# Kernel tuning notes

Measured on AMD Instinct MI355X. Metric: run time of the kernel, lower is better.

Reference implementation:

```python
import jax, jax.numpy as jnp
import numpy as np

N = 25000        # nodes
E = 400000       # edges (avg degree 16)
F = 128          # num_features
NRBF = 20        # num_rbf_features
CUTOFF = 5.0


def setup_inputs() -> dict:
    key = jax.random.key(0)
    ks = jax.random.split(key, 9)
    node_scalar = jax.random.normal(ks[0], (N, F), jnp.float32)
    node_vector = jax.random.normal(ks[1], (N, F, 3), jnp.float32)
    dst = jax.random.randint(ks[2], (E,), 0, N)
    src = jax.random.randint(ks[3], (E,), 0, N)
    r = jax.random.normal(ks[4], (E, 3), jnp.float32) * 1.5
    d = jnp.clip(jnp.linalg.norm(r, axis=-1), 0.1, None)
    adj_matrix = jnp.concatenate(
        [dst[:, None].astype(jnp.float32), src[:, None].astype(jnp.float32), r, d[:, None]],
        axis=-1)  # [E, 6]
    s_in = 1.0 / np.sqrt(F)
    s_rbf = 1.0 / np.sqrt(NRBF)
    W1 = jax.random.normal(ks[5], (F, F), jnp.float32) * s_in
    b1 = jnp.zeros((F,), jnp.float32)
    W2 = jax.random.normal(ks[6], (F, 3 * F), jnp.float32) * s_in
    b2 = jnp.zeros((3 * F,), jnp.float32)
    Wr = jax.random.normal(ks[7], (NRBF, 3 * F), jnp.float32) * s_rbf
    br = jnp.zeros((3 * F,), jnp.float32)
    return dict(node_scalar=node_scalar, node_vector=node_vector, adj_matrix=adj_matrix,
                W1=W1, b1=b1, W2=W2, b2=b2, Wr=Wr, br=br)


def reference(node_scalar, node_vector, adj_matrix, W1, b1, W2, b2, Wr, br):
    # scalar message MLP: Linear -> SiLU -> Linear, [N, 3F]
    atom_scalar = jax.nn.silu(node_scalar @ W1 + b1) @ W2 + b2

    dst = adj_matrix[:, 0].astype(jnp.int32)
    src = adj_matrix[:, 1].astype(jnp.int32)
    r_ij = adj_matrix[:, 2:5]              # [E, 3]
    d = adj_matrix[:, 5]                   # [E]

    # sinc expansion: sin(d * n * pi / cutoff) / d, n = 1..NRBF -> [E, NRBF]
    n_vals = jnp.arange(1, NRBF + 1, dtype=jnp.float32)
    sinc = jnp.sin(d[:, None] * n_vals * jnp.pi / CUTOFF) / d[:, None]
    rbf = sinc @ Wr + br                   # [E, 3F]
    cut = jnp.where(d < CUTOFF, 0.5 * (jnp.cos(jnp.pi * d / CUTOFF) + 1.0), 0.0)
    w = rbf * cut[:, None]                 # [E, 3F]

    pre_split = atom_scalar[src] * w       # [E, 3F]
    s1, s2, s3 = jnp.split(pre_split, 3, axis=-1)  # each [E, F]

    r_hat = r_ij / d[:, None]              # [E, 3]
    # message_vector: [E, F, 3]
    message_vector = node_vector[src] * s1[:, :, None] + s3[:, :, None] * r_hat[:, None, :]

    delta_s = jnp.zeros_like(node_scalar).at[dst].add(s2)
    delta_v = jnp.zeros_like(node_vector).at[dst].add(message_vector)
    return node_scalar + delta_s, node_vector + delta_v
```

## Files before the change

### kernel.cpp

```cpp
#include <hip/hip_runtime.h>

#define FDIM 128
#define NRBF 20
constexpr float CUTOFF_F = 5.0f;
constexpr float PI_F = 3.14159265358979323846f;

typedef _Float16 h2 __attribute__((ext_vector_type(2)));
typedef _Float16 half4 __attribute__((ext_vector_type(4)));
typedef float f32x4 __attribute__((ext_vector_type(4)));

__device__ __forceinline__ uint packh(float a, float b) {
  union { _Float16 h[2]; uint u; } x;
  x.h[0] = (_Float16)a;
  x.h[1] = (_Float16)b;
  return x.u;
}
__device__ __forceinline__ float h_lo(uint w) {
  union { uint u; _Float16 h[2]; } x;
  x.u = w;
  return (float)x.h[0];
}
__device__ __forceinline__ float h_hi(uint w) {
  union { uint u; _Float16 h[2]; } x;
  x.u = w;
  return (float)x.h[1];
}
__device__ __forceinline__ float dot2(uint cw, h2 w, float acc) {
#if __has_builtin(__builtin_amdgcn_fdot2)
  h2 c = __builtin_bit_cast(h2, cw);
  return __builtin_amdgcn_fdot2(c, w, acc, false);
#else
  return fmaf(h_hi(cw), (float)w[1], fmaf(h_lo(cw), (float)w[0], acc));
#endif
}

__global__ __launch_bounds__(256) void wconv2(const float* __restrict__ W1,
                                              const float* __restrict__ W2,
                                              _Float16* __restrict__ w1h,
                                              _Float16* __restrict__ w2h) {
  int idx = blockIdx.x * blockDim.x + threadIdx.x;
  const float* W;
  _Float16* outp;
  int NC, NCOLS, base;
  if (idx < 8 * 8 * 256) {
    W = W1; outp = w1h; NC = 8; NCOLS = 128; base = idx;
  } else if (idx < 8 * 8 * 256 + 8 * 24 * 256) {
    W = W2; outp = w2h; NC = 24; NCOLS = 384; base = idx - 8 * 8 * 256;
  } else {
    return;
  }
  int i = base & 3;
  int l = (base >> 2) & 63;
  int rem = base >> 8;
  int c = rem % NC, s = rem / NC;
  int k = s * 16 + ((l >> 4) & 3) * 4 + i;
  int col = c * 16 + (l & 15);
  outp[base] = (_Float16)W[(size_t)k * NCOLS + col];
}

__global__ __launch_bounds__(256) void gemm_fused(
    const float* __restrict__ A, const half4* __restrict__ w1h,
    const float* __restrict__ b1, const half4* __restrict__ w2h,
    const float* __restrict__ b2, const float* __restrict__ nvec,
    uint* __restrict__ bundle, int M) {
  __shared__ _Float16 Ah[64][136];
  const int t = threadIdx.x;
  const int w = t >> 6;
  const int l = t & 63;
  const int lr = l & 15, lg = (l >> 4) & 3;
  const int row0 = blockIdx.x * 64;

  for (int i = t; i < 64 * 32; i += 256) {
    int r = i >> 5, c4 = (i & 31) << 2;
    int gr = row0 + r;
    float4 v = make_float4(0.f, 0.f, 0.f, 0.f);
    if (gr < M) v = *(const float4*)&A[(size_t)gr * FDIM + c4];
    half4 hv = {(_Float16)v.x, (_Float16)v.y, (_Float16)v.z, (_Float16)v.w};
    *(half4*)&Ah[r][c4] = hv;
  }
  __syncthreads();

  half4 af[8];
#pragma unroll
  for (int s = 0; s < 8; ++s)
    af[s] = *(const half4*)&Ah[16 * w + lr][s * 16 + lg * 4];

  f32x4 acc1[8];
#pragma unroll
  for (int c = 0; c < 8; ++c) acc1[c] = {0.f, 0.f, 0.f, 0.f};
#pragma unroll
  for (int s = 0; s < 8; ++s) {
#pragma unroll
    for (int c = 0; c < 8; ++c) {
      half4 bf = w1h[(s * 8 + c) * 64 + l];
      acc1[c] = __builtin_amdgcn_mfma_f32_16x16x16f16(af[s], bf, acc1[c], 0, 0, 0);
    }
  }
  __syncthreads();
#pragma unroll
  for (int c = 0; c < 8; ++c) {
    float bb = b1[c * 16 + lr];
#pragma unroll
    for (int r = 0; r < 4; ++r) {
      float x = acc1[c][r] + bb;
      x = x / (1.f + __expf(-x));
      Ah[16 * w + lg * 4 + r][c * 16 + lr] = (_Float16)x;
    }
  }
  __syncthreads();

  half4 hf[8];
#pragma unroll
  for (int s = 0; s < 8; ++s)
    hf[s] = *(const half4*)&Ah[16 * w + lr][s * 16 + lg * 4];

#pragma unroll 1
  for (int cg = 0; cg < 8; ++cg) {
    f32x4 a3[3];
#pragma unroll
    for (int p = 0; p < 3; ++p) a3[p] = {0.f, 0.f, 0.f, 0.f};
#pragma unroll
    for (int s = 0; s < 8; ++s) {
#pragma unroll
      for (int p = 0; p < 3; ++p) {
        half4 bf = w2h[(s * 24 + cg + p * 8) * 64 + l];
        a3[p] = __builtin_amdgcn_mfma_f32_16x16x16f16(hf[s], bf, a3[p], 0, 0, 0);
      }
    }
    const int j = cg * 16 + lr;
    const float bb0 = b2[j], bb1 = b2[j + 128], bb2 = b2[j + 256];
#pragma unroll
    for (int r = 0; r < 4; ++r) {
      int n = row0 + 16 * w + lg * 4 + r;
      if (n >= M) continue;
      const float* vb = nvec + ((size_t)n * FDIM + j) * 3;
      float v0 = vb[0], v1 = vb[1], v2 = vb[2];
      uint* o = bundle + ((size_t)n * FDIM + j) * 3;
      o[0] = packh(a3[0][r] + bb0, a3[1][r] + bb1);
      o[1] = packh(a3[2][r] + bb2, v0);
      o[2] = packh(v1, v2);
    }
  }
}

__global__ __launch_bounds__(256) void hist_kernel(const float* __restrict__ adj,
                                                   int* __restrict__ counts,
                                                   int E) {
  int e = blockIdx.x * blockDim.x + threadIdx.x;
  if (e < E) atomicAdd(&counts[(int)adj[(size_t)e * 6]], 1);
}

__global__ __launch_bounds__(1024) void scan_kernel(
    const int* __restrict__ counts, int* __restrict__ offs,
    int* __restrict__ cursor, int n) {
  __shared__ int part[1024];
  const int tid = threadIdx.x;
  const int CH = (n + 1023) >> 10;
  const int b = tid * CH;
  const int e = min(b + CH, n);
  int s = 0;
  for (int i = b; i < e; ++i) s += counts[i];
  part[tid] = s;
  __syncthreads();
  for (int off = 1; off < 1024; off <<= 1) {
    int v = (tid >= off) ? part[tid - off] : 0;
    __syncthreads();
    part[tid] += v;
    __syncthreads();
  }
  int run = part[tid] - s;
  if (tid == 0) offs[0] = 0;
  for (int i = b; i < e; ++i) {
    int c = counts[i];
    cursor[i] = run;
    run += c;
    offs[i + 1] = run;
  }
}

__global__ __launch_bounds__(256) void edge_prep(const float* __restrict__ adj,
                                                 int* __restrict__ cursor,
                                                 int* __restrict__ eids,
                                                 uint* __restrict__ rec, int E) {
  int e = blockIdx.x * blockDim.x + threadIdx.x;
  if (e >= E) return;
  const float* a = adj + (size_t)e * 6;
  int dst = (int)a[0];
  int src = (int)a[1];
  float rx = a[2], ry = a[3], rz = a[4], d = a[5];

  int p = atomicAdd(&cursor[dst], 1);
  eids[p] = e;

  float x = d * (PI_F / CUTOFF_F);
  float sx, cx;
  __sincosf(x, &sx, &cx);
  float invd = 1.f / d;
  float cut = (d < CUTOFF_F) ? 0.5f * (cx + 1.f) : 0.f;
  float sc = invd * cut;

  union { uint w[14]; uint2 q[7]; } R;
  R.w[0] = (uint)src;
  R.w[1] = packh(rx * invd, ry * invd);
  R.w[2] = packh(rz * invd, cut);
  float twoc = 2.f * cx;
  float sprev = 0.f, scur = sx;
  float c[NRBF];
#pragma unroll
  for (int n = 0; n < NRBF; ++n) {
    c[n] = scur * sc;
    float nxt = fmaf(twoc, scur, -sprev);
    sprev = scur;
    scur = nxt;
  }
#pragma unroll
  for (int m = 0; m < 10; ++m) R.w[3 + m] = packh(c[2 * m], c[2 * m + 1]);
  R.w[13] = 0;
  uint2* o = (uint2*)(rec + (size_t)p * 14);
#pragma unroll
  for (int m = 0; m < 7; ++m) o[m] = R.q[m];
}

__global__ __launch_bounds__(128) void accum_kernel(
    const uint* __restrict__ rec, const uint* __restrict__ bundle,
    const float* __restrict__ nvec, const float* __restrict__ Wr,
    const float* __restrict__ br, const float* __restrict__ ns,
    const int* __restrict__ offs, const int* __restrict__ eids,
    float* __restrict__ out_s, float* __restrict__ out_v, int Nn) {
  const int j = threadIdx.x;

  h2 wp0[10], wp1[10], wp2[10];
#pragma unroll
  for (int m = 0; m < 10; ++m) {
    wp0[m] = h2{(_Float16)Wr[(2 * m) * 384 + j], (_Float16)Wr[(2 * m + 1) * 384 + j]};
    wp1[m] = h2{(_Float16)Wr[(2 * m) * 384 + 128 + j], (_Float16)Wr[(2 * m + 1) * 384 + 128 + j]};
    wp2[m] = h2{(_Float16)Wr[(2 * m) * 384 + 256 + j], (_Float16)Wr[(2 * m + 1) * 384 + 256 + j]};
  }
  const float brj0 = br[j], brj1 = br[j + 128], brj2 = br[j + 256];

  __shared__ int sh_e[128], sh_pos[128];

#define SLOT(t) ((t) < 128 ? sh_pos[(t)] : (t))
#define LOADREC(R, t)                                                      \
  {                                                                        \
    int su = __builtin_amdgcn_readfirstlane(beg + SLOT(t));                \
    const uint* p = rec + (size_t)(uint)su * 14;                           \
    _Pragma("unroll") for (int w_ = 0; w_ < 13; ++w_) R[w_] = p[w_];       \
  }
#define LOADB(B0, B1, B2, SRC)                                             \
  {                                                                        \
    const uint* p = bundle + ((size_t)(uint)(SRC)*FDIM + j) * 3;           \
    B0 = p[0];                                                             \
    B1 = p[1];                                                             \
    B2 = p[2];                                                             \
  }

  for (int d = blockIdx.x; d < Nn; d += gridDim.x) {
    const int beg = offs[d];
    const int cnt = offs[d + 1] - beg;
    const int m = cnt < 128 ? cnt : 128;
    if (j < m) sh_e[j] = eids[beg + j];
    __syncthreads();
    if (j < m) {
      int v = sh_e[j];
      int r = 0;
      for (int u = 0; u < m; ++u) r += (sh_e[u] < v);
      sh_pos[r] = j;
    }
    __syncthreads();

    float acc_s = 0.f, av0 = 0.f, av1 = 0.f, av2 = 0.f;

    uint r_cur[13], r_nxt[13];
    uint b0 = 0, b1 = 0, b2 = 0;
    if (cnt > 0) LOADREC(r_cur, 0);
    if (cnt > 1) LOADREC(r_nxt, 1);
    if (cnt > 0) LOADB(b0, b1, b2, (int)r_cur[0]);

    for (int t = 0; t < cnt; ++t) {
      uint nb0 = 0, nb1 = 0, nb2 = 0;
      if (t + 1 < cnt) LOADB(nb0, nb1, nb2, (int)r_nxt[0]);
      uint r_n2[13];
      if (t + 2 < cnt) LOADREC(r_n2, t + 2);

      float rhx = h_lo(r_cur[1]), rhy = h_hi(r_cur[1]);
      float rhz = h_lo(r_cur[2]), cut = h_hi(r_cur[2]);
      float w0 = cut * brj0, w1 = cut * brj1, w2 = cut * brj2;
#pragma unroll
      for (int q = 0; q < 10; ++q) {
        w0 = dot2(r_cur[3 + q], wp0[q], w0);
        w1 = dot2(r_cur[3 + q], wp1[q], w1);
        w2 = dot2(r_cur[3 + q], wp2[q], w2);
      }
      float s1 = h_lo(b0) * w0;
      float s2 = h_hi(b0) * w1;
      float s3 = h_lo(b1) * w2;
      float pv0 = h_hi(b1), pv1 = h_lo(b2), pv2 = h_hi(b2);
      acc_s += s2;
      av0 = fmaf(pv0, s1, fmaf(s3, rhx, av0));
      av1 = fmaf(pv1, s1, fmaf(s3, rhy, av1));
      av2 = fmaf(pv2, s1, fmaf(s3, rhz, av2));

#pragma unroll
      for (int w_ = 0; w_ < 13; ++w_) {
        r_cur[w_] = r_nxt[w_];
        r_nxt[w_] = r_n2[w_];
      }
      b0 = nb0;
      b1 = nb1;
      b2 = nb2;
    }

    out_s[(size_t)d * FDIM + j] = ns[(size_t)d * FDIM + j] + acc_s;
    float* vo = out_v + (size_t)d * 384 + j * 3;
    const float* vi = nvec + (size_t)d * 384 + j * 3;
    vo[0] = vi[0] + av0;
    vo[1] = vi[1] + av1;
    vo[2] = vi[2] + av2;
  }
#undef SLOT
#undef LOADREC
#undef LOADB
}

extern "C" void kernel_launch(void* const* d_in, const int* in_sizes, int n_in,
                              void* d_out, int out_size, void* d_ws,
                              size_t ws_size, hipStream_t stream) {
  const float* node_scalar = (const float*)d_in[0];
  const float* node_vector = (const float*)d_in[1];
  const float* adj = (const float*)d_in[2];
  const float* W1 = (const float*)d_in[3];
  const float* b1 = (const float*)d_in[4];
  const float* W2 = (const float*)d_in[5];
  const float* b2 = (const float*)d_in[6];
  const float* Wr = (const float*)d_in[7];
  const float* br = (const float*)d_in[8];

  const int N = in_sizes[0] / FDIM;
  const int E = in_sizes[2] / 6;

  float* out = (float*)d_out;
  float* out_s = out;
  float* out_v = out + (size_t)N * FDIM;

  char* w = (char*)d_ws;
  uint* bundle = (uint*)w;
  size_t off = (size_t)N * FDIM * 12;
  uint* rec = (uint*)(w + off);
  off += (size_t)E * 56;
  _Float16* w1h = (_Float16*)(w + off);
  off += 8 * 8 * 256 * 2;
  _Float16* w2h = (_Float16*)(w + off);
  off += 8 * 24 * 256 * 2;
  int* counts = (int*)(w + off);
  int* offs = counts + N;
  int* cursor = offs + N + 1;
  int* eids = cursor + N;

  hipMemsetAsync(counts, 0, (size_t)N * sizeof(int), stream);
  hist_kernel<<<(E + 255) / 256, 256, 0, stream>>>(adj, counts, E);
  scan_kernel<<<1, 1024, 0, stream>>>(counts, offs, cursor, N);
  edge_prep<<<(E + 255) / 256, 256, 0, stream>>>(adj, cursor, eids, rec, E);

  wconv2<<<(8 * 8 * 256 + 8 * 24 * 256 + 255) / 256, 256, 0, stream>>>(
      W1, W2, w1h, w2h);
  gemm_fused<<<(N + 63) / 64, 256, 0, stream>>>(node_scalar, (const half4*)w1h,
                                                b1, (const half4*)w2h, b2,
                                                node_vector, bundle, N);

  const int agrid = N < 4096 ? N : 4096;
  accum_kernel<<<agrid, 128, 0, stream>>>(rec, bundle, node_vector, Wr, br,
                                          node_scalar, offs, eids, out_s,
                                          out_v, N);
}
```

Baseline: 285.1 us.

## Deepen bundle prefetch via shared src list and fold counts memset into wconv2

The accumulation kernel now stores each edge's source index in shared memory during the sort step. Bundle loads therefore no longer wait on the previous record load, and they are prefetched three edges ahead instead of one. Edges beyond the first 128 per node go through a separate unpipelined fallback loop. The hipMemsetAsync that zeroes the degree counts is folded into the weight-conversion kernel, which now launches first, saving one stream operation. The cost is more registers for the extra prefetch buffers and an additional shared array.

```diff
diff --git a/kernel.cpp b/kernel.cpp
--- a/kernel.cpp
+++ b/kernel.cpp
@@ -34,11 +34,16 @@
 #endif
 }
 
+struct Bun { uint x, y, z; };
+
 __global__ __launch_bounds__(256) void wconv2(const float* __restrict__ W1,
                                               const float* __restrict__ W2,
                                               _Float16* __restrict__ w1h,
-                                              _Float16* __restrict__ w2h) {
+                                              _Float16* __restrict__ w2h,
+                                              int* __restrict__ counts,
+                                              int Ncnt) {
   int idx = blockIdx.x * blockDim.x + threadIdx.x;
+  if (idx < Ncnt) counts[idx] = 0;
   const float* W;
   _Float16* outp;
   int NC, NCOLS, base;
@@ -238,21 +243,40 @@
   }
   const float brj0 = br[j], brj1 = br[j + 128], brj2 = br[j + 256];
 
-  __shared__ int sh_e[128], sh_pos[128];
-
-#define SLOT(t) ((t) < 128 ? sh_pos[(t)] : (t))
+  __shared__ int sh_e[128], sh_pos[128], sh_src[128];
+
 #define LOADREC(R, t)                                                      \
   {                                                                        \
-    int su = __builtin_amdgcn_readfirstlane(beg + SLOT(t));                \
+    int su = __builtin_amdgcn_readfirstlane(beg + sh_pos[(t)]);            \
     const uint* p = rec + (size_t)(uint)su * 14;                           \
     _Pragma("unroll") for (int w_ = 0; w_ < 13; ++w_) R[w_] = p[w_];       \
   }
-#define LOADB(B0, B1, B2, SRC)                                             \
+#define LOADB(B, tt)                                                       \
   {                                                                        \
-    const uint* p = bundle + ((size_t)(uint)(SRC)*FDIM + j) * 3;           \
-    B0 = p[0];                                                             \
-    B1 = p[1];                                                             \
-    B2 = p[2];                                                             \
+    int su = __builtin_amdgcn_readfirstlane(sh_src[(tt)]);                 \
+    const uint* p = bundle + ((size_t)(uint)su * FDIM + j) * 3;            \
+    (B).x = p[0];                                                          \
+    (B).y = p[1];                                                          \
+    (B).z = p[2];                                                          \
+  }
+#define COMPUTE(RC, BB)                                                    \
+  {                                                                        \
+    float rhx = h_lo(RC[1]), rhy = h_hi(RC[1]);                            \
+    float rhz = h_lo(RC[2]), cut = h_hi(RC[2]);                            \
+    float w0 = cut * brj0, w1 = cut * brj1, w2 = cut * brj2;               \
+    _Pragma("unroll") for (int q = 0; q < 10; ++q) {                       \
+      w0 = dot2(RC[3 + q], wp0[q], w0);                                    \
+      w1 = dot2(RC[3 + q], wp1[q], w1);                                    \
+      w2 = dot2(RC[3 + q], wp2[q], w2);                                    \
+    }                                                                      \
+    float s1 = h_lo((BB).x) * w0;                                          \
+    float s2 = h_hi((BB).x) * w1;                                          \
+    float s3 = h_lo((BB).y) * w2;                                          \
+    float pv0 = h_hi((BB).y), pv1 = h_lo((BB).z), pv2 = h_hi((BB).z);      \
+    acc_s += s2;                                                           \
+    av0 = fmaf(pv0, s1, fmaf(s3, rhx, av0));                               \
+    av1 = fmaf(pv1, s1, fmaf(s3, rhy, av1));                               \
+    av2 = fmaf(pv2, s1, fmaf(s3, rhz, av2));                               \
   }
 
   for (int d = blockIdx.x; d < Nn; d += gridDim.x) {
@@ -266,49 +290,51 @@
       int r = 0;
       for (int u = 0; u < m; ++u) r += (sh_e[u] < v);
       sh_pos[r] = j;
+      sh_src[r] = (int)rec[(size_t)(uint)(beg + j) * 14];
     }
     __syncthreads();
 
     float acc_s = 0.f, av0 = 0.f, av1 = 0.f, av2 = 0.f;
 
     uint r_cur[13], r_nxt[13];
-    uint b0 = 0, b1 = 0, b2 = 0;
-    if (cnt > 0) LOADREC(r_cur, 0);
-    if (cnt > 1) LOADREC(r_nxt, 1);
-    if (cnt > 0) LOADB(b0, b1, b2, (int)r_cur[0]);
-
-    for (int t = 0; t < cnt; ++t) {
-      uint nb0 = 0, nb1 = 0, nb2 = 0;
-      if (t + 1 < cnt) LOADB(nb0, nb1, nb2, (int)r_nxt[0]);
+    Bun b0_ = {}, b1_ = {}, b2_ = {}, b3_ = {};
+    if (m > 0) { LOADB(b0_, 0); LOADREC(r_cur, 0); }
+    if (m > 1) { LOADB(b1_, 1); LOADREC(r_nxt, 1); }
+    if (m > 2) LOADB(b2_, 2);
+
+    for (int t = 0; t < m; ++t) {
+      if (t + 3 < m) LOADB(b3_, t + 3);
       uint r_n2[13];
-      if (t + 2 < cnt) LOADREC(r_n2, t + 2);
-
-      float rhx = h_lo(r_cur[1]), rhy = h_hi(r_cur[1]);
-      float rhz = h_lo(r_cur[2]), cut = h_hi(r_cur[2]);
-      float w0 = cut * brj0, w1 = cut * brj1, w2 = cut * brj2;
-#pragma unroll
-      for (int q = 0; q < 10; ++q) {
-        w0 = dot2(r_cur[3 + q], wp0[q], w0);
-        w1 = dot2(r_cur[3 + q], wp1[q], w1);
-        w2 = dot2(r_cur[3 + q], wp2[q], w2);
-      }
-      float s1 = h_lo(b0) * w0;
-      float s2 = h_hi(b0) * w1;
-      float s3 = h_lo(b1) * w2;
-      float pv0 = h_hi(b1), pv1 = h_lo(b2), pv2 = h_hi(b2);
-      acc_s += s2;
-      av0 = fmaf(pv0, s1, fmaf(s3, rhx, av0));
-      av1 = fmaf(pv1, s1, fmaf(s3, rhy, av1));
-      av2 = fmaf(pv2, s1, fmaf(s3, rhz, av2));
+      if (t + 2 < m) LOADREC(r_n2, t + 2);
+
+      COMPUTE(r_cur, b0_);
 
 #pragma unroll
       for (int w_ = 0; w_ < 13; ++w_) {
         r_cur[w_] = r_nxt[w_];
         r_nxt[w_] = r_n2[w_];
       }
-      b0 = nb0;
-      b1 = nb1;
-      b2 = nb2;
+      b0_ = b1_;
+      b1_ = b2_;
+      b2_ = b3_;
+    }
+
+    for (int t = 128; t < cnt; ++t) {
+      uint R[13];
+      {
+        int su = __builtin_amdgcn_readfirstlane(beg + t);
+        const uint* p = rec + (size_t)(uint)su * 14;
+#pragma unroll
+        for (int w_ = 0; w_ < 13; ++w_) R[w_] = p[w_];
+      }
+      Bun Bx;
+      {
+        const uint* p = bundle + ((size_t)(uint)R[0] * FDIM + j) * 3;
+        Bx.x = p[0];
+        Bx.y = p[1];
+        Bx.z = p[2];
+      }
+      COMPUTE(R, Bx);
     }
 
     out_s[(size_t)d * FDIM + j] = ns[(size_t)d * FDIM + j] + acc_s;
@@ -318,9 +344,9 @@
     vo[1] = vi[1] + av1;
     vo[2] = vi[2] + av2;
   }
-#undef SLOT
 #undef LOADREC
 #undef LOADB
+#undef COMPUTE
 }
 
 extern "C" void kernel_launch(void* const* d_in, const int* in_sizes, int n_in,
@@ -357,13 +383,12 @@
   int* cursor = offs + N + 1;
   int* eids = cursor + N;
 
-  hipMemsetAsync(counts, 0, (size_t)N * sizeof(int), stream);
+  wconv2<<<(8 * 8 * 256 + 8 * 24 * 256 + 255) / 256, 256, 0, stream>>>(
+      W1, W2, w1h, w2h, counts, N);
   hist_kernel<<<(E + 255) / 256, 256, 0, stream>>>(adj, counts, E);
   scan_kernel<<<1, 1024, 0, stream>>>(counts, offs, cursor, N);
   edge_prep<<<(E + 255) / 256, 256, 0, stream>>>(adj, cursor, eids, rec, E);
 
-  wconv2<<<(8 * 8 * 256 + 8 * 24 * 256 + 255) / 256, 256, 0, stream>>>(
-      W1, W2, w1h, w2h);
   gemm_fused<<<(N + 63) / 64, 256, 0, stream>>>(node_scalar, (const half4*)w1h,
                                                 b1, (const half4*)w2h, b2,
                                                 node_vector, bundle, N);
```

Result: slower. 320.4 us (+12.4%).
